# Performance work log

Hardware: AMD Instinct MI355X
Metric: run time of the kernel (lower is better)

Reference implementation:

```python
import jax, jax.numpy as jnp
import numpy as np
from jax.scipy.special import logsumexp

N = 4096          # nodes per graph
E = 65536         # edges per graph
HID = 128
HEADS = 4
HD = HID // HEADS
L_GNN = 2
L_CROSS = 3
SINK_ITERS = 20
LN_EPS = 1e-5
SCALE = 1.0 / np.sqrt(HD)


def layer_norm(x, g, b):
    m = jnp.mean(x, axis=-1, keepdims=True)
    v = jnp.mean((x - m) ** 2, axis=-1, keepdims=True)
    return (x - m) * jax.lax.rsqrt(v + LN_EPS) * g + b


def gcn_conv(x, ei, w, b):
    # PyG GCNConv: self-loops + symmetric normalization, sum aggregation
    n = x.shape[0]
    xl = x @ w                                  # [n, hid]
    loops = jnp.arange(n, dtype=ei.dtype)
    src = jnp.concatenate([ei[0], loops])
    dst = jnp.concatenate([ei[1], loops])
    deg = jax.ops.segment_sum(jnp.ones_like(src, dtype=x.dtype), dst, num_segments=n)
    dinv = jnp.where(deg > 0, jax.lax.rsqrt(deg), 0.0)
    norm = dinv[src] * dinv[dst]                # [E+n]
    msg = xl[src] * norm[:, None]
    return jax.ops.segment_sum(msg, dst, num_segments=n) + b


def encode(x, ei, gcn_w, gcn_b, ln_g, ln_b):
    h = x
    for l in range(L_GNN):
        h = gcn_conv(h, ei, gcn_w[l], gcn_b[l])
        h = layer_norm(h, ln_g[l], ln_b[l])
        h = jax.nn.relu(h)
    return h


def attend(X, Y, wq, wk, wv, wo, bo):
    # X attends to Y; residual add
    n, m = X.shape[0], Y.shape[0]
    Q = (X @ wq).reshape(n, HEADS, HD).transpose(1, 0, 2)   # [h, n, d]
    K = (Y @ wk).reshape(m, HEADS, HD).transpose(1, 0, 2)
    V = (Y @ wv).reshape(m, HEADS, HD).transpose(1, 0, 2)
    scores = jnp.einsum('hnd,hmd->hnm', Q, K) * SCALE
    attn = jax.nn.softmax(scores, axis=-1)
    O = jnp.einsum('hnm,hmd->hnd', attn, V)                 # [h, n, d]
    O = O.transpose(1, 0, 2).reshape(n, HID)
    return O @ wo + bo + X


def sinkhorn(log_alpha, n_iters=SINK_ITERS):
    def body(i, lp):
        lp = lp - logsumexp(lp, axis=1, keepdims=True)  # row normalize
        lp = lp - logsumexp(lp, axis=0, keepdims=True)  # col normalize
        return lp
    log_p = jax.lax.fori_loop(0, n_iters, body, log_alpha)
    return jnp.exp(log_p)


def setup_inputs() -> dict:
    key = jax.random.key(0)
    ks = jax.random.split(key, 24)
    f32 = jnp.float32
    w = lambda k, *s: jax.random.normal(k, s, dtype=f32) * 0.05
    inp = {
        'A_x': jax.random.normal(ks[0], (N, HID), dtype=f32),
        'A_ei': jax.random.randint(ks[1], (2, E), 0, N),
        'B_x': jax.random.normal(ks[2], (N, HID), dtype=f32),
        'B_ei': jax.random.randint(ks[3], (2, E), 0, N),
        'in_proj_w': w(ks[4], HID, HID),
        'in_proj_b': jnp.zeros((HID,), f32),
        'gcn_w': w(ks[5], L_GNN, HID, HID),
        'gcn_b': jnp.zeros((L_GNN, HID), f32),
        'gcn_ln_g': jnp.ones((L_GNN, HID), f32),
        'gcn_ln_b': jnp.zeros((L_GNN, HID), f32),
        'cross_q': w(ks[6], L_CROSS, HID, HID),
        'cross_k': w(ks[7], L_CROSS, HID, HID),
        'cross_v': w(ks[8], L_CROSS, HID, HID),
        'cross_o': w(ks[9], L_CROSS, HID, HID),
        'cross_o_b': jnp.zeros((L_CROSS, HID), f32),
        'post_ln_g': jnp.ones((HID,), f32),
        'post_ln_b': jnp.zeros((HID,), f32),
        'proj_w': w(ks[10], HID, HID),
        'proj_b': jnp.zeros((HID,), f32),
        'null_vec': jax.random.normal(ks[11], (HID,), dtype=f32) * 0.01,
        'cp_w1': w(ks[12], HID, HID),
        'cp_b1': jnp.zeros((HID,), f32),
        'cp_w2': w(ks[13], HID, HID),
        'cp_b2': jnp.zeros((HID,), f32),
    }
    return inp


def reference(A_x, A_ei, B_x, B_ei, in_proj_w, in_proj_b, gcn_w, gcn_b,
              gcn_ln_g, gcn_ln_b, cross_q, cross_k, cross_v, cross_o,
              cross_o_b, post_ln_g, post_ln_b, proj_w, proj_b, null_vec,
              cp_w1, cp_b1, cp_w2, cp_b2):
    A_in = A_x @ in_proj_w + in_proj_b
    B_in = B_x @ in_proj_w + in_proj_b
    A_h = encode(A_in, A_ei, gcn_w, gcn_b, gcn_ln_g, gcn_ln_b)
    B_h = encode(B_in, B_ei, gcn_w, gcn_b, gcn_ln_g, gcn_ln_b)
    for l in range(L_CROSS):
        A_new = attend(A_h, B_h, cross_q[l], cross_k[l], cross_v[l], cross_o[l], cross_o_b[l])
        B_new = attend(B_h, A_h, cross_q[l], cross_k[l], cross_v[l], cross_o[l], cross_o_b[l])
        A_h, B_h = A_new, B_new
    A_h = layer_norm(A_h, post_ln_g, post_ln_b)
    B_h = layer_norm(B_h, post_ln_g, post_ln_b)
    A_p = A_h @ proj_w + proj_b
    B_p = B_h @ proj_w + proj_b
    inv_sqrt_d = 1.0 / np.sqrt(HID)
    logits = (A_p @ B_p.T) * inv_sqrt_d                    # [N, N]
    null_col = (A_p @ null_vec) * inv_sqrt_d               # [N]
    logits_with_null = jnp.concatenate([logits, null_col[:, None]], axis=1)
    P = sinkhorn(logits_with_null)
    zA = jax.nn.relu(A_p @ cp_w1 + cp_b1) @ cp_w2 + cp_b2
    zB = jax.nn.relu(B_p @ cp_w1 + cp_b1) @ cp_w2 + cp_b2
    return (logits_with_null, P, zA, zB)
```

## Files before the change

kernel.cpp:

```cpp
#include <hip/hip_runtime.h>
#include <hip/hip_bf16.h>
#include <math.h>

#define NN 4096
#define EE 65536
#define HID_ 128
#define HDIM 32
#define NCOL 4097
#define EHP 4104

static constexpr float SCALE_ATT = 0.17677669529663687f;
static constexpr float INV_SQRT_D = 0.08838834764831845f;
static constexpr float LOG2E = 1.4426950408889634f;

typedef __attribute__((ext_vector_type(8))) short bf16x8;
typedef __attribute__((ext_vector_type(4))) float f32x4;
typedef _Float16 half8 __attribute__((ext_vector_type(8)));
typedef _Float16 half4v __attribute__((ext_vector_type(4)));

__device__ __forceinline__ float wred64(float v) {
#pragma unroll
  for (int m = 32; m > 0; m >>= 1) v += __shfl_xor(v, m, 64);
  return v;
}

__device__ __forceinline__ ushort f2b(float f) {
  __hip_bfloat16 h = __float2bfloat16(f);
  union { __hip_bfloat16 h; ushort u; } c;
  c.h = h;
  return c.u;
}

__device__ __forceinline__ unsigned pack2bf(float e0, float e1) {
  return ((__float_as_uint(e1) + 0x8000u) & 0xffff0000u) |
         ((__float_as_uint(e0) + 0x8000u) >> 16);
}

__global__ void wprep_k(const float* __restrict__ in_w,
                        const float* __restrict__ gcn_w,
                        const float* __restrict__ cq,
                        const float* __restrict__ ck,
                        const float* __restrict__ cv,
                        const float* __restrict__ co,
                        const float* __restrict__ pw,
                        const float* __restrict__ w1,
                        const float* __restrict__ w2, ushort* __restrict__ wth,
                        ushort* __restrict__ wtl) {
  int s = blockIdx.y;
  const float* W = s == 0    ? in_w
                   : s < 3   ? gcn_w + (size_t)(s - 1) * 16384
                   : s < 6   ? cq + (size_t)(s - 3) * 16384
                   : s < 9   ? ck + (size_t)(s - 6) * 16384
                   : s < 12  ? cv + (size_t)(s - 9) * 16384
                   : s < 15  ? co + (size_t)(s - 12) * 16384
                   : s == 15 ? pw
                   : s == 16 ? w1
                             : w2;
  int n0 = blockIdx.x * 16;
  int tid = threadIdx.x;
#pragma unroll
  for (int i = 0; i < 8; ++i) {
    int idx = tid + i * 256;
    int k = idx & 127, nn = idx >> 7;
    float v = W[(size_t)k * 128 + n0 + nn];
    ushort h = f2b(v);
    float hf = __uint_as_float((unsigned)h << 16);
    ushort lo = f2b(v - hf);
    size_t o = (size_t)s * 16384 + (size_t)(n0 + nn) * 128 + k;
    wth[o] = h;
    wtl[o] = lo;
  }
}

template <bool BIAS, bool RELU, bool RESID, bool BF16OUT, bool COMBINE>
__global__ __launch_bounds__(256) void gemm_mfma_k(
    const float* __restrict__ x0, const float* __restrict__ x1,
    const float* __restrict__ lp, const ushort* __restrict__ wth,
    const ushort* __restrict__ wtl, const float* __restrict__ bias,
    const float* __restrict__ res0, const float* __restrict__ res1,
    float* __restrict__ o0, float* __restrict__ o1, ushort* __restrict__ ob0,
    ushort* __restrict__ ob1) {
  __shared__ ushort Xh[32 * 128], Xl[32 * 128];
  __shared__ ushort Whs[64 * 128], Wls[64 * 128];
  const int tid = threadIdx.x;
  const int dir = blockIdx.y;
  const int m0 = blockIdx.x * 32;
  const float* res = dir ? res1 : res0;
  float* out = dir ? o1 : o0;
  ushort* outb = dir ? ob1 : ob0;

  {
    const float* x = dir ? x1 : x0;
#pragma unroll
    for (int i = 0; i < 2; ++i) {
      int c = tid + i * 256;
      int row = c >> 4, ch = c & 15;
      int rowg = m0 + row;
      float v[8];
      if (COMBINE) {
        int hh = ch >> 2;
        float ls = lp[((size_t)(dir * 4 + hh)) * NN + rowg] +
                   lp[((size_t)((2 + dir) * 4 + hh)) * NN + rowg];
        float inv = 1.f / ls;
        const float* p0 = &x0[((size_t)dir * NN + rowg) * HID_ + ch * 8];
        const float* p1 = &x0[((size_t)(2 + dir) * NN + rowg) * HID_ + ch * 8];
        float4 a0 = *(const float4*)p0, a1 = *(const float4*)(p0 + 4);
        float4 b0 = *(const float4*)p1, b1 = *(const float4*)(p1 + 4);
        v[0] = (a0.x + b0.x) * inv; v[1] = (a0.y + b0.y) * inv;
        v[2] = (a0.z + b0.z) * inv; v[3] = (a0.w + b0.w) * inv;
        v[4] = (a1.x + b1.x) * inv; v[5] = (a1.y + b1.y) * inv;
        v[6] = (a1.z + b1.z) * inv; v[7] = (a1.w + b1.w) * inv;
      } else {
        float4 a0 = *(const float4*)&x[(size_t)rowg * HID_ + ch * 8];
        float4 a1 = *(const float4*)&x[(size_t)rowg * HID_ + ch * 8 + 4];
        v[0] = a0.x; v[1] = a0.y; v[2] = a0.z; v[3] = a0.w;
        v[4] = a1.x; v[5] = a1.y; v[6] = a1.z; v[7] = a1.w;
      }
      union { ushort u[8]; bf16x8 vv; } H, L;
#pragma unroll
      for (int e = 0; e < 8; ++e) {
        ushort h = f2b(v[e]);
        float hf = __uint_as_float((unsigned)h << 16);
        H.u[e] = h;
        L.u[e] = f2b(v[e] - hf);
      }
      int pch = ch ^ (row & 15);
      *(bf16x8*)&Xh[row * 128 + pch * 8] = H.vv;
      *(bf16x8*)&Xl[row * 128 + pch * 8] = L.vv;
    }
  }

  const int w = tid >> 6, l = tid & 63, lr = l & 15, lg = l >> 4;
  const int mrow = (w & 1) * 16 + lr;
  const int nb = (w >> 1) * 2;

#pragma unroll
  for (int nh = 0; nh < 2; ++nh) {
    if (nh) __syncthreads();
#pragma unroll
    for (int i = 0; i < 4; ++i) {
      int c = tid + i * 256;
      int row = c >> 4, ch = c & 15;
      int pch = ch ^ (row & 15);
      *(bf16x8*)&Whs[row * 128 + pch * 8] =
          *(const bf16x8*)&wth[(size_t)(nh * 64 + row) * 128 + ch * 8];
      *(bf16x8*)&Wls[row * 128 + pch * 8] =
          *(const bf16x8*)&wtl[(size_t)(nh * 64 + row) * 128 + ch * 8];
    }
    __syncthreads();
    f32x4 acc0 = {0.f, 0.f, 0.f, 0.f}, acc1 = {0.f, 0.f, 0.f, 0.f};
#pragma unroll
    for (int kc = 0; kc < 4; ++kc) {
      int chx = ((kc * 4 + lg) ^ lr) * 8;
      bf16x8 ah = *(const bf16x8*)&Xh[mrow * 128 + chx];
      bf16x8 al = *(const bf16x8*)&Xl[mrow * 128 + chx];
      bf16x8 bh0 = *(const bf16x8*)&Whs[(nb * 16 + lr) * 128 + chx];
      bf16x8 bl0 = *(const bf16x8*)&Wls[(nb * 16 + lr) * 128 + chx];
      bf16x8 bh1 = *(const bf16x8*)&Whs[((nb + 1) * 16 + lr) * 128 + chx];
      bf16x8 bl1 = *(const bf16x8*)&Wls[((nb + 1) * 16 + lr) * 128 + chx];
      acc0 = __builtin_amdgcn_mfma_f32_16x16x32_bf16(ah, bh0, acc0, 0, 0, 0);
      acc0 = __builtin_amdgcn_mfma_f32_16x16x32_bf16(al, bh0, acc0, 0, 0, 0);
      acc0 = __builtin_amdgcn_mfma_f32_16x16x32_bf16(ah, bl0, acc0, 0, 0, 0);
      acc1 = __builtin_amdgcn_mfma_f32_16x16x32_bf16(ah, bh1, acc1, 0, 0, 0);
      acc1 = __builtin_amdgcn_mfma_f32_16x16x32_bf16(al, bh1, acc1, 0, 0, 0);
      acc1 = __builtin_amdgcn_mfma_f32_16x16x32_bf16(ah, bl1, acc1, 0, 0, 0);
    }
#pragma unroll
    for (int j = 0; j < 2; ++j) {
      const f32x4 a = j ? acc1 : acc0;
      int col = nh * 64 + (nb + j) * 16 + lr;
      float bv = BIAS ? bias[col] : 0.f;
#pragma unroll
      for (int r = 0; r < 4; ++r) {
        int rowg = m0 + (w & 1) * 16 + lg * 4 + r;
        float val = a[r] + bv;
        if (RESID) val += res[(size_t)rowg * HID_ + col];
        if (RELU) val = fmaxf(val, 0.f);
        out[(size_t)rowg * HID_ + col] = val;
        if (BF16OUT) outb[(size_t)rowg * HID_ + col] = f2b(val);
      }
    }
  }
}

__global__ __launch_bounds__(256) void gemm_qkv_mfma_k(
    const float* __restrict__ x0, const float* __restrict__ x1,
    const ushort* __restrict__ wthQ, const ushort* __restrict__ wtlQ,
    const ushort* __restrict__ wthK, const ushort* __restrict__ wtlK,
    const ushort* __restrict__ wthV, const ushort* __restrict__ wtlV,
    ushort* __restrict__ QA, ushort* __restrict__ QB, ushort* __restrict__ KA,
    ushort* __restrict__ KB, ushort* __restrict__ VA,
    ushort* __restrict__ VB) {
  __shared__ ushort Xh[32 * 128], Xl[32 * 128];
  __shared__ ushort Whs[64 * 128], Wls[64 * 128];
  const int tid = threadIdx.x;
  const int dir = blockIdx.y, z = blockIdx.z;
  const int m0 = blockIdx.x * 32;
  const ushort* wth = z == 0 ? wthQ : (z == 1 ? wthK : wthV);
  const ushort* wtl = z == 0 ? wtlQ : (z == 1 ? wtlK : wtlV);
  ushort* out = z == 0 ? (dir ? QB : QA)
                       : (z == 1 ? (dir ? KB : KA) : (dir ? VB : VA));
  const float scale = (z == 0) ? SCALE_ATT * LOG2E : 1.f;
  {
    const float* x = dir ? x1 : x0;
#pragma unroll
    for (int i = 0; i < 2; ++i) {
      int c = tid + i * 256;
      int row = c >> 4, ch = c & 15;
      int rowg = m0 + row;
      float4 a0 = *(const float4*)&x[(size_t)rowg * HID_ + ch * 8];
      float4 a1 = *(const float4*)&x[(size_t)rowg * HID_ + ch * 8 + 4];
      float v[8] = {a0.x, a0.y, a0.z, a0.w, a1.x, a1.y, a1.z, a1.w};
      union { ushort u[8]; bf16x8 vv; } H, L;
#pragma unroll
      for (int e = 0; e < 8; ++e) {
        ushort h = f2b(v[e]);
        float hf = __uint_as_float((unsigned)h << 16);
        H.u[e] = h;
        L.u[e] = f2b(v[e] - hf);
      }
      int pch = ch ^ (row & 15);
      *(bf16x8*)&Xh[row * 128 + pch * 8] = H.vv;
      *(bf16x8*)&Xl[row * 128 + pch * 8] = L.vv;
    }
  }
  const int w = tid >> 6, l = tid & 63, lr = l & 15, lg = l >> 4;
  const int mrow = (w & 1) * 16 + lr;
  const int nb = (w >> 1) * 2;
#pragma unroll
  for (int nh = 0; nh < 2; ++nh) {
    if (nh) __syncthreads();
#pragma unroll
    for (int i = 0; i < 4; ++i) {
      int c = tid + i * 256;
      int row = c >> 4, ch = c & 15;
      int pch = ch ^ (row & 15);
      *(bf16x8*)&Whs[row * 128 + pch * 8] =
          *(const bf16x8*)&wth[(size_t)(nh * 64 + row) * 128 + ch * 8];
      *(bf16x8*)&Wls[row * 128 + pch * 8] =
          *(const bf16x8*)&wtl[(size_t)(nh * 64 + row) * 128 + ch * 8];
    }
    __syncthreads();
    f32x4 acc0 = {0.f, 0.f, 0.f, 0.f}, acc1 = {0.f, 0.f, 0.f, 0.f};
#pragma unroll
    for (int kc = 0; kc < 4; ++kc) {
      int chx = ((kc * 4 + lg) ^ lr) * 8;
      bf16x8 ah = *(const bf16x8*)&Xh[mrow * 128 + chx];
      bf16x8 al = *(const bf16x8*)&Xl[mrow * 128 + chx];
      bf16x8 bh0 = *(const bf16x8*)&Whs[(nb * 16 + lr) * 128 + chx];
      bf16x8 bl0 = *(const bf16x8*)&Wls[(nb * 16 + lr) * 128 + chx];
      bf16x8 bh1 = *(const bf16x8*)&Whs[((nb + 1) * 16 + lr) * 128 + chx];
      bf16x8 bl1 = *(const bf16x8*)&Wls[((nb + 1) * 16 + lr) * 128 + chx];
      acc0 = __builtin_amdgcn_mfma_f32_16x16x32_bf16(ah, bh0, acc0, 0, 0, 0);
      acc0 = __builtin_amdgcn_mfma_f32_16x16x32_bf16(al, bh0, acc0, 0, 0, 0);
      acc0 = __builtin_amdgcn_mfma_f32_16x16x32_bf16(ah, bl0, acc0, 0, 0, 0);
      acc1 = __builtin_amdgcn_mfma_f32_16x16x32_bf16(ah, bh1, acc1, 0, 0, 0);
      acc1 = __builtin_amdgcn_mfma_f32_16x16x32_bf16(al, bh1, acc1, 0, 0, 0);
      acc1 = __builtin_amdgcn_mfma_f32_16x16x32_bf16(ah, bl1, acc1, 0, 0, 0);
    }
#pragma unroll
    for (int j = 0; j < 2; ++j) {
      const f32x4 a = j ? acc1 : acc0;
      int col = nh * 64 + (nb + j) * 16 + lr;
#pragma unroll
      for (int r = 0; r < 4; ++r) {
        int rowg = m0 + (w & 1) * 16 + lg * 4 + r;
        if (z < 2)
          out[(size_t)rowg * HID_ + col] = f2b(a[r] * scale);
        else
          out[(size_t)col * NN + rowg] = f2b(a[r]);
      }
    }
  }
}

__global__ void count_deg_k(const int* __restrict__ eiA,
                            const int* __restrict__ eiB, int* cntA, int* cntB) {
  int e = blockIdx.x * 256 + threadIdx.x;
  const int* ei = blockIdx.y ? eiB : eiA;
  int* cnt = blockIdx.y ? cntB : cntA;
  atomicAdd(&cnt[ei[EE + e]], 1);
}

__global__ __launch_bounds__(1024) void scan_k(const int* cntA, const int* cntB,
                                               int* rpA, int* rpB, float* dinvA,
                                               float* dinvB) {
  const int* cnt = blockIdx.y ? cntB : cntA;
  int* rp = blockIdx.y ? rpB : rpA;
  float* dinv = blockIdx.y ? dinvB : dinvA;
  __shared__ int part[1024];
  int tid = threadIdx.x;
  int v0 = cnt[tid * 4], v1 = cnt[tid * 4 + 1], v2 = cnt[tid * 4 + 2],
      v3 = cnt[tid * 4 + 3];
  int tot = v0 + v1 + v2 + v3;
  part[tid] = tot;
  __syncthreads();
  int x = tot;
  for (int off = 1; off < 1024; off <<= 1) {
    int y = (tid >= off) ? part[tid - off] : 0;
    __syncthreads();
    x += y;
    part[tid] = x;
    __syncthreads();
  }
  int excl = x - tot;
  rp[tid * 4] = excl;
  rp[tid * 4 + 1] = excl + v0;
  rp[tid * 4 + 2] = excl + v0 + v1;
  rp[tid * 4 + 3] = excl + v0 + v1 + v2;
  if (tid == 1023) rp[4096] = x;
  dinv[tid * 4] = rsqrtf((float)(v0 + 1));
  dinv[tid * 4 + 1] = rsqrtf((float)(v1 + 1));
  dinv[tid * 4 + 2] = rsqrtf((float)(v2 + 1));
  dinv[tid * 4 + 3] = rsqrtf((float)(v3 + 1));
}

__global__ void fill_k(const int* __restrict__ eiA, const int* __restrict__ eiB,
                       const int* rpA, const int* rpB, int* fillA, int* fillB,
                       int* srcA, int* srcB) {
  int e = blockIdx.x * 256 + threadIdx.x;
  const int* ei = blockIdx.y ? eiB : eiA;
  const int* rp = blockIdx.y ? rpB : rpA;
  int* fill = blockIdx.y ? fillB : fillA;
  int* src = blockIdx.y ? srcB : srcA;
  int d = ei[EE + e], s = ei[e];
  int pos = atomicAdd(&fill[d], 1);
  src[rp[d] + pos] = s;
}

__global__ __launch_bounds__(256) void gcn_agg_k(
    const float* __restrict__ xlA, const float* __restrict__ xlB,
    const int* __restrict__ rpA, const int* __restrict__ rpB,
    const int* __restrict__ srcA, const int* __restrict__ srcB,
    const float* __restrict__ dinvA, const float* __restrict__ dinvB,
    const float* __restrict__ gb, const float* __restrict__ lg,
    const float* __restrict__ lb, float* __restrict__ outA,
    float* __restrict__ outB) {
  const float* xl = blockIdx.y ? xlB : xlA;
  const int* rp = blockIdx.y ? rpB : rpA;
  const int* src = blockIdx.y ? srcB : srcA;
  const float* dinv = blockIdx.y ? dinvB : dinvA;
  float* out = blockIdx.y ? outB : outA;
  int wid = threadIdx.x >> 6, lane = threadIdx.x & 63;
  int node = blockIdx.x * 4 + wid;
  int b = rp[node], e = rp[node + 1];
  float di = dinv[node];
  float a0 = 0.f, a1 = 0.f;
  for (int base = b; base < e; base += 64) {
    int rem = e - base;
    int sv = 0;
    float wv = 0.f;
    if (lane < rem) {
      int s = src[base + lane];
      sv = s;
      wv = dinv[s] * di;
    }
    int nch = rem < 64 ? rem : 64;
    for (int j = 0; j < nch; ++j) {
      int s = __shfl(sv, j, 64);
      float w = __shfl(wv, j, 64);
      a0 += xl[(size_t)s * HID_ + lane] * w;
      a1 += xl[(size_t)s * HID_ + 64 + lane] * w;
    }
  }
  a0 += xl[(size_t)node * HID_ + lane] * di * di;
  a1 += xl[(size_t)node * HID_ + 64 + lane] * di * di;
  a0 += gb[lane];
  a1 += gb[64 + lane];
  float mean = wred64(a0 + a1) * (1.f / 128.f);
  float d0 = a0 - mean, d1 = a1 - mean;
  float var = wred64(d0 * d0 + d1 * d1) * (1.f / 128.f);
  float rs = rsqrtf(var + 1e-5f);
  float o0 = d0 * rs * lg[lane] + lb[lane];
  float o1 = d1 * rs * lg[64 + lane] + lb[64 + lane];
  out[(size_t)node * HID_ + lane] = fmaxf(o0, 0.f);
  out[(size_t)node * HID_ + 64 + lane] = fmaxf(o1, 0.f);
}

__global__ __launch_bounds__(256) void ln_k(float* __restrict__ hA,
                                            float* __restrict__ hB,
                                            const float* __restrict__ g,
                                            const float* __restrict__ b) {
  float* h = blockIdx.y ? hB : hA;
  int wid = threadIdx.x >> 6, lane = threadIdx.x & 63;
  int row = blockIdx.x * 4 + wid;
  float a0 = h[(size_t)row * HID_ + lane];
  float a1 = h[(size_t)row * HID_ + 64 + lane];
  float mean = wred64(a0 + a1) * (1.f / 128.f);
  float d0 = a0 - mean, d1 = a1 - mean;
  float var = wred64(d0 * d0 + d1 * d1) * (1.f / 128.f);
  float rs = rsqrtf(var + 1e-5f);
  h[(size_t)row * HID_ + lane] = d0 * rs * g[lane] + b[lane];
  h[(size_t)row * HID_ + 64 + lane] = d1 * rs * g[64 + lane] + b[64 + lane];
}

__global__ __launch_bounds__(256, 4) void attn_mfma_k(
    const ushort* __restrict__ QA, const ushort* __restrict__ KA,
    const ushort* __restrict__ VtA, const ushort* __restrict__ QB,
    const ushort* __restrict__ KB, const ushort* __restrict__ VtB,
    float* __restrict__ Opart, float* __restrict__ lpart) {
  const int qt = blockIdx.x, h = blockIdx.y;
  const int dir = blockIdx.z >> 1, sl = blockIdx.z & 1;
  const ushort* Q = dir ? QB : QA;
  const ushort* K = dir ? KA : KB;
  const ushort* Vt = dir ? VtA : VtB;

  __shared__ ushort KF[2048];
  __shared__ ushort VF[2048];
  __shared__ ushort PF[4][1024];

  const int tid = threadIdx.x;
  const int w = tid >> 6, l = tid & 63;
  const int lr = l & 15, lg = l >> 4;

  const int qrow = qt * 64 + w * 16 + lr;
  bf16x8 qf = *(const bf16x8*)&Q[(size_t)qrow * HID_ + h * HDIM + lg * 8];

  f32x4 oacc0 = {0.f, 0.f, 0.f, 0.f};
  f32x4 oacc1 = {0.f, 0.f, 0.f, 0.f};
  float lsum = 0.f;

  const int ldst = ((w * 4 + lg) * 16 + lr) * 8;
  const ushort* Kg =
      K + (size_t)(sl * 2048 + w * 16 + lr) * HID_ + h * HDIM + lg * 8;
  const ushort* Vg = Vt + (size_t)(h * HDIM + (w >> 1) * 16 + lr) * NN +
                     sl * 2048 + (w & 1) * 32 + lg * 8;

  bf16x8 kreg = *(const bf16x8*)Kg;
  bf16x8 vreg = *(const bf16x8*)Vg;

  for (int t = 0; t < 32; ++t) {
    __syncthreads();
    *(bf16x8*)&KF[ldst] = kreg;
    *(bf16x8*)&VF[ldst] = vreg;
    if (t < 31) {
      kreg = *(const bf16x8*)&Kg[(size_t)(t + 1) * 64 * HID_];
      vreg = *(const bf16x8*)&Vg[(t + 1) * 64];
    }
    __syncthreads();
#pragma unroll
    for (int s = 0; s < 4; ++s) {
      bf16x8 kf = *(const bf16x8*)&KF[((s * 4 + lg) * 16 + lr) * 8];
      f32x4 c = {0.f, 0.f, 0.f, 0.f};
      c = __builtin_amdgcn_mfma_f32_16x16x32_bf16(kf, qf, c, 0, 0, 0);
      float e0 = exp2f(c[0]), e1 = exp2f(c[1]);
      float e2 = exp2f(c[2]), e3 = exp2f(c[3]);
      lsum += (e0 + e1) + (e2 + e3);
      const int k0 = s >> 1;
      const int lgr = (s & 1) * 2 + (lg >> 1);
      const int e8 = (lg & 1) * 4;
      *(uint2*)&PF[w][((k0 * 4 + lgr) * 16 + lr) * 8 + e8] =
          make_uint2(pack2bf(e0, e1), pack2bf(e2, e3));
    }
#pragma unroll
    for (int k0 = 0; k0 < 2; ++k0) {
      bf16x8 pa = *(const bf16x8*)&PF[w][((k0 * 4 + lg) * 16 + lr) * 8];
      bf16x8 vb0 = *(const bf16x8*)&VF[((k0 * 4 + lg) * 16 + lr) * 8];
      bf16x8 vb1 = *(const bf16x8*)&VF[(((2 + k0) * 4 + lg) * 16 + lr) * 8];
      oacc0 = __builtin_amdgcn_mfma_f32_16x16x32_bf16(pa, vb0, oacc0, 0, 0, 0);
      oacc1 = __builtin_amdgcn_mfma_f32_16x16x32_bf16(pa, vb1, oacc1, 0, 0, 0);
    }
  }
  lsum += __shfl_xor(lsum, 16, 64);
  lsum += __shfl_xor(lsum, 32, 64);
  const int pb = sl * 2 + dir;
  if (lg == 0)
    lpart[(size_t)(pb * 4 + h) * NN + qt * 64 + w * 16 + lr] = lsum;
#pragma unroll
  for (int r = 0; r < 4; ++r) {
    int q = qt * 64 + w * 16 + lg * 4 + r;
    Opart[((size_t)pb * NN + q) * HID_ + h * HDIM + lr] = oacc0[r];
    Opart[((size_t)pb * NN + q) * HID_ + h * HDIM + 16 + lr] = oacc1[r];
  }
}

__global__ __launch_bounds__(256, 2) void gemm_nt_mfma_k(
    const ushort* __restrict__ Apb, const ushort* __restrict__ Bpb,
    float* __restrict__ L, _Float16* __restrict__ Eh) {
  __shared__ ushort As[128 * 128];
  __shared__ ushort Bs[128 * 128];
  const int tid = threadIdx.x;
  const int ab = blockIdx.y * 128, bb = blockIdx.x * 128;
#pragma unroll
  for (int i = 0; i < 8; ++i) {
    int lin = tid + i * 256;
    int row = lin >> 4, ch = lin & 15;
    int pch = ch ^ (row & 15);
    *(bf16x8*)&As[row * 128 + pch * 8] =
        *(const bf16x8*)&Apb[(size_t)(ab + row) * HID_ + ch * 8];
    *(bf16x8*)&Bs[row * 128 + pch * 8] =
        *(const bf16x8*)&Bpb[(size_t)(bb + row) * HID_ + ch * 8];
  }
  __syncthreads();
  const int w = tid >> 6, l = tid & 63, lr = l & 15, lg = l >> 4;
  f32x4 acc[2][8];
#pragma unroll
  for (int fm = 0; fm < 2; ++fm)
#pragma unroll
    for (int nf = 0; nf < 8; ++nf) acc[fm][nf] = {0.f, 0.f, 0.f, 0.f};
#pragma unroll
  for (int kc = 0; kc < 4; ++kc) {
    bf16x8 a0 = *(const bf16x8*)
        &As[((w * 2 + 0) * 16 + lr) * 128 + ((kc * 4 + lg) ^ lr) * 8];
    bf16x8 a1 = *(const bf16x8*)
        &As[((w * 2 + 1) * 16 + lr) * 128 + ((kc * 4 + lg) ^ lr) * 8];
#pragma unroll
    for (int nf = 0; nf < 8; ++nf) {
      bf16x8 bf = *(const bf16x8*)
          &Bs[(nf * 16 + lr) * 128 + ((kc * 4 + lg) ^ lr) * 8];
      acc[0][nf] = __builtin_amdgcn_mfma_f32_16x16x32_bf16(a0, bf, acc[0][nf], 0, 0, 0);
      acc[1][nf] = __builtin_amdgcn_mfma_f32_16x16x32_bf16(a1, bf, acc[1][nf], 0, 0, 0);
    }
  }
#pragma unroll
  for (int fm = 0; fm < 2; ++fm)
#pragma unroll
    for (int nf = 0; nf < 8; ++nf)
#pragma unroll
      for (int r = 0; r < 4; ++r) {
        int row = ab + (w * 2 + fm) * 16 + lg * 4 + r;
        int col = bb + nf * 16 + lr;
        float v = acc[fm][nf][r] * INV_SQRT_D;
        L[(size_t)row * NCOL + col] = v;
        Eh[(size_t)row * EHP + col] = (_Float16)exp2f(v * LOG2E);
      }
}

__global__ void null_col_k(const float* __restrict__ Ap,
                           const float* __restrict__ nv, float* __restrict__ L,
                           _Float16* __restrict__ Eh) {
  int row = blockIdx.x, lane = threadIdx.x;
  float s = Ap[(size_t)row * HID_ + lane] * nv[lane] +
            Ap[(size_t)row * HID_ + 64 + lane] * nv[64 + lane];
  s = wred64(s);
  if (lane == 0) {
    float v = s * INV_SQRT_D;
    L[(size_t)row * NCOL + 4096] = v;
    Eh[(size_t)row * EHP + 4096] = (_Float16)exp2f(v * LOG2E);
  }
  if (lane >= 1 && lane < 8) Eh[(size_t)row * EHP + 4096 + lane] = (_Float16)0.f;
}

__global__ __launch_bounds__(256) void sink_fused_k(
    const _Float16* __restrict__ Eh, const float* __restrict__ t_old,
    float* __restrict__ t_new, float* __restrict__ colpart,
    float* __restrict__ u) {
  __shared__ float vinv[EHP];
  __shared__ float uls[16];
  const int tid = threadIdx.x, bid = blockIdx.x;
  if (bid < 17) {
    int z = bid * 256 + tid;
    if (z < EHP) t_new[z] = 0.f;
  }
  for (int i = tid; i < EHP; i += 256)
    vinv[i] = (i < NCOL) ? (1.f / t_old[i]) : 0.f;
  __syncthreads();
  const int w = tid >> 6, l = tid & 63;
  const int row0 = bid * 16;
#pragma unroll
  for (int rr = 0; rr < 4; ++rr) {
    int row = row0 + w * 4 + rr;
    const _Float16* Ep = Eh + (size_t)row * EHP;
    float s = 0.f;
    for (int j = l * 4; j < EHP; j += 256) {
      half4v e = *(const half4v*)&Ep[j];
      float4 vv = *(const float4*)&vinv[j];
      s += (float)e[0] * vv.x + (float)e[1] * vv.y + (float)e[2] * vv.z +
           (float)e[3] * vv.w;
    }
    s = wred64(s);
    if (l == 0) {
      float uv = 1.f / s;
      uls[w * 4 + rr] = uv;
      u[row] = uv;
    }
  }
  __syncthreads();
  float ur[16];
#pragma unroll
  for (int r = 0; r < 16; ++r) ur[r] = uls[r];
  float* cp = colpart + (size_t)bid * EHP;
  for (int j = tid * 4; j < EHP; j += 1024) {
    float a0 = 0.f, a1 = 0.f, a2 = 0.f, a3 = 0.f;
#pragma unroll
    for (int r = 0; r < 16; ++r) {
      half4v e = *(const half4v*)&Eh[(size_t)(row0 + r) * EHP + j];
      a0 += (float)e[0] * ur[r];
      a1 += (float)e[1] * ur[r];
      a2 += (float)e[2] * ur[r];
      a3 += (float)e[3] * ur[r];
    }
    *(float4*)&cp[j] = make_float4(a0, a1, a2, a3);
  }
}

__global__ __launch_bounds__(256) void sink_reduce_k(
    const float* __restrict__ colpart, float* __restrict__ t_new) {
  int j = blockIdx.x * 256 + threadIdx.x;
  if (j >= EHP) return;
  int b0 = blockIdx.y * 32;
  float s = 0.f;
#pragma unroll 8
  for (int b = 0; b < 32; ++b) s += colpart[(size_t)(b0 + b) * EHP + j];
  atomicAdd(&t_new[j], s);
}

__global__ void sink_init_k(float* t0) {
  int j = blockIdx.x * 256 + threadIdx.x;
  if (j < EHP) t0[j] = 1.f;
}

__global__ __launch_bounds__(256) void sink_finalE_k(
    const _Float16* __restrict__ Eh, const float* __restrict__ u,
    const float* __restrict__ t, float* __restrict__ P) {
  __shared__ float vls[NCOL];
  int tid = threadIdx.x, row = blockIdx.x;
  for (int i = tid; i < NCOL; i += 256) vls[i] = 1.f / t[i];
  __syncthreads();
  float ur = u[row];
  const _Float16* Ep = Eh + (size_t)row * EHP;
  float* Pp = P + (size_t)row * NCOL;
  for (int j = tid; j < NCOL; j += 256) Pp[j] = (float)Ep[j] * ur * vls[j];
}

extern "C" void kernel_launch(void* const* d_in, const int* in_sizes, int n_in,
                              void* d_out, int out_size, void* d_ws,
                              size_t ws_size, hipStream_t stream) {
  const float* A_x = (const float*)d_in[0];
  const int* A_ei = (const int*)d_in[1];
  const float* B_x = (const float*)d_in[2];
  const int* B_ei = (const int*)d_in[3];
  const float* in_w = (const float*)d_in[4];
  const float* in_b = (const float*)d_in[5];
  const float* gcn_w = (const float*)d_in[6];
  const float* gcn_b = (const float*)d_in[7];
  const float* lng = (const float*)d_in[8];
  const float* lnb = (const float*)d_in[9];
  const float* cq = (const float*)d_in[10];
  const float* ck = (const float*)d_in[11];
  const float* cv = (const float*)d_in[12];
  const float* co = (const float*)d_in[13];
  const float* cob = (const float*)d_in[14];
  const float* plg = (const float*)d_in[15];
  const float* plb = (const float*)d_in[16];
  const float* pw = (const float*)d_in[17];
  const float* pb = (const float*)d_in[18];
  const float* nullv = (const float*)d_in[19];
  const float* w1 = (const float*)d_in[20];
  const float* b1 = (const float*)d_in[21];
  const float* w2 = (const float*)d_in[22];
  const float* b2 = (const float*)d_in[23];

  float* ws = (float*)d_ws;
  size_t off = 0;
  auto alloc = [&](size_t n) { float* p = ws + off; off += n; return p; };
  const size_t NHE = (size_t)NN * HID_;
  float* tA = alloc(NHE);
  float* tB = alloc(NHE);
  float* Ap = alloc(NHE);
  float* Bp = alloc(NHE);
  ushort* Apb = (ushort*)alloc(NHE / 2);
  ushort* Bpb = (ushort*)alloc(NHE / 2);
  ushort* WThi = (ushort*)alloc((size_t)18 * 16384 / 2);
  ushort* WTlo = (ushort*)alloc((size_t)18 * 16384 / 2);
  float* uvec = alloc(NN);
  float* t0 = alloc(EHP);
  float* t1 = alloc(EHP);
  float* zone = ws + off;
  float* hA0 = alloc(NHE); float* hB0 = alloc(NHE);
  float* hA1 = alloc(NHE); float* hB1 = alloc(NHE);
  float* QA = alloc(NHE);  float* KAb = alloc(NHE); float* VAb = alloc(NHE);
  float* QB = alloc(NHE);  float* KBb = alloc(NHE); float* VBb = alloc(NHE);
  float* Opart = alloc(4 * NHE);
  float* lpart = alloc((size_t)16 * NN);
  float* dinvA = alloc(NN); float* dinvB = alloc(NN);
  int* ib = (int*)(ws + off);
  int* cntA = ib;             int* cntB = cntA + NN;
  int* fillA = cntB + NN;     int* fillB = fillA + NN;
  int* rpA = fillB + NN;      int* rpB = rpA + (NN + 1);
  int* srcA = rpB + (NN + 1); int* srcB = srcA + EE;
  size_t ints_floats = (size_t)(4 * NN + 2 * (NN + 1) + 2 * EE);
  _Float16* Eh = (_Float16*)zone;
  {
    size_t named = (size_t)((ws + off) - zone) + ints_floats;
    size_t eh_floats = ((size_t)NN * EHP + 1) / 2;
    size_t need = eh_floats > named ? eh_floats : named;
    off = (size_t)(zone - ws) + need;
  }
  float* colpart = alloc((size_t)256 * EHP);

  float* Lout = (float*)d_out;
  float* Pout = Lout + (size_t)NN * NCOL;
  float* zA = Pout + (size_t)NN * NCOL;
  float* zB = zA + NHE;

  hipMemsetAsync(cntA, 0, 4 * NN * sizeof(int), stream);

  wprep_k<<<dim3(8, 18), 256, 0, stream>>>(in_w, gcn_w, cq, ck, cv, co, pw, w1,
                                           w2, WThi, WTlo);
  gemm_mfma_k<true, false, false, false, false>
      <<<dim3(128, 2), 256, 0, stream>>>(A_x, B_x, nullptr, WThi, WTlo, in_b,
                                         nullptr, nullptr, hA0, hB0, nullptr,
                                         nullptr);
  count_deg_k<<<dim3(256, 2), 256, 0, stream>>>(A_ei, B_ei, cntA, cntB);
  scan_k<<<dim3(1, 2), 1024, 0, stream>>>(cntA, cntB, rpA, rpB, dinvA, dinvB);
  fill_k<<<dim3(256, 2), 256, 0, stream>>>(A_ei, B_ei, rpA, rpB, fillA, fillB,
                                           srcA, srcB);
  float* hA = hA0; float* hB = hB0; float* aA = hA1; float* aB = hB1;
  for (int l = 0; l < 2; ++l) {
    gemm_mfma_k<false, false, false, false, false>
        <<<dim3(128, 2), 256, 0, stream>>>(
            hA, hB, nullptr, WThi + (size_t)16384 * (1 + l),
            WTlo + (size_t)16384 * (1 + l), nullptr, nullptr, nullptr, tA, tB,
            nullptr, nullptr);
    gcn_agg_k<<<dim3(1024, 2), 256, 0, stream>>>(
        tA, tB, rpA, rpB, srcA, srcB, dinvA, dinvB, gcn_b + l * HID_,
        lng + l * HID_, lnb + l * HID_, hA, hB);
  }
  for (int l = 0; l < 3; ++l) {
    gemm_qkv_mfma_k<<<dim3(128, 2, 3), 256, 0, stream>>>(
        hA, hB, WThi + (size_t)16384 * (3 + l), WTlo + (size_t)16384 * (3 + l),
        WThi + (size_t)16384 * (6 + l), WTlo + (size_t)16384 * (6 + l),
        WThi + (size_t)16384 * (9 + l), WTlo + (size_t)16384 * (9 + l),
        (ushort*)QA, (ushort*)QB, (ushort*)KAb, (ushort*)KBb, (ushort*)VAb,
        (ushort*)VBb);
    attn_mfma_k<<<dim3(64, 4, 4), 256, 0, stream>>>(
        (ushort*)QA, (ushort*)KAb, (ushort*)VAb, (ushort*)QB, (ushort*)KBb,
        (ushort*)VBb, Opart, lpart);
    gemm_mfma_k<true, false, true, false, true>
        <<<dim3(128, 2), 256, 0, stream>>>(
            Opart, nullptr, lpart, WThi + (size_t)16384 * (12 + l),
            WTlo + (size_t)16384 * (12 + l), cob + l * HID_, hA, hB, aA, aB,
            nullptr, nullptr);
    float* t;
    t = hA; hA = aA; aA = t;
    t = hB; hB = aB; aB = t;
  }
  ln_k<<<dim3(1024, 2), 256, 0, stream>>>(hA, hB, plg, plb);
  gemm_mfma_k<true, false, false, true, false>
      <<<dim3(128, 2), 256, 0, stream>>>(hA, hB, nullptr,
                                         WThi + (size_t)16384 * 15,
                                         WTlo + (size_t)16384 * 15, pb, nullptr,
                                         nullptr, Ap, Bp, Apb, Bpb);
  gemm_nt_mfma_k<<<dim3(32, 32), 256, 0, stream>>>(Apb, Bpb, Lout, Eh);
  null_col_k<<<NN, 64, 0, stream>>>(Ap, nullv, Lout, Eh);
  sink_init_k<<<17, 256, 0, stream>>>(t0);
  float* tb[2] = {t0, t1};
  for (int it = 0; it < 20; ++it) {
    float* told = tb[it & 1];
    float* tnew = tb[(it + 1) & 1];
    sink_fused_k<<<256, 256, 0, stream>>>(Eh, told, tnew, colpart, uvec);
    sink_reduce_k<<<dim3(17, 8), 256, 0, stream>>>(colpart, tnew);
  }
  sink_finalE_k<<<NN, 256, 0, stream>>>(Eh, uvec, tb[0], Pout);
  gemm_mfma_k<true, true, false, false, false>
      <<<dim3(128, 2), 256, 0, stream>>>(Ap, Bp, nullptr,
                                         WThi + (size_t)16384 * 16,
                                         WTlo + (size_t)16384 * 16, b1, nullptr,
                                         nullptr, tA, tB, nullptr, nullptr);
  gemm_mfma_k<true, false, false, false, false>
      <<<dim3(128, 2), 256, 0, stream>>>(tA, tB, nullptr,
                                         WThi + (size_t)16384 * 17,
                                         WTlo + (size_t)16384 * 17, b2, nullptr,
                                         nullptr, zA, zB, nullptr, nullptr);
}
```

Before: 1.079 ms.

## Fuse Sinkhorn column reduction via replicated atomics and widen attention key split

Each Sinkhorn iteration now uses one kernel instead of two. Column sums are accumulated with atomics into 8 replicated accumulator buffers, rotated through three buffers so one can be zeroed while the others are read. This removes the colpart staging buffer and the separate reduce launch, at the cost of atomic contention and readers summing 8 replicas. Attention splits the key range into 4 slices instead of 2, with a higher occupancy hint to add parallelism, and the combine step sums 4 partials. The bf16 hi/lo split is also rewritten with integer rounding arithmetic.

```diff
diff --git a/kernel.cpp b/kernel.cpp
--- a/kernel.cpp
+++ b/kernel.cpp
@@ -8,6 +8,7 @@
 #define HDIM 32
 #define NCOL 4097
 #define EHP 4104
+#define NREP 8
 
 static constexpr float SCALE_ATT = 0.17677669529663687f;
 static constexpr float INV_SQRT_D = 0.08838834764831845f;
@@ -15,7 +16,6 @@
 
 typedef __attribute__((ext_vector_type(8))) short bf16x8;
 typedef __attribute__((ext_vector_type(4))) float f32x4;
-typedef _Float16 half8 __attribute__((ext_vector_type(8)));
 typedef _Float16 half4v __attribute__((ext_vector_type(4)));
 
 __device__ __forceinline__ float wred64(float v) {
@@ -34,6 +34,13 @@
 __device__ __forceinline__ unsigned pack2bf(float e0, float e1) {
   return ((__float_as_uint(e1) + 0x8000u) & 0xffff0000u) |
          ((__float_as_uint(e0) + 0x8000u) >> 16);
+}
+
+__device__ __forceinline__ void split2(float v, ushort& h, ushort& l) {
+  unsigned hb = (__float_as_uint(v) + 0x8000u) & 0xffff0000u;
+  h = (ushort)(hb >> 16);
+  float lo = v - __uint_as_float(hb);
+  l = (ushort)((__float_as_uint(lo) + 0x8000u) >> 16);
 }
 
 __global__ void wprep_k(const float* __restrict__ in_w,
@@ -63,9 +70,8 @@
     int idx = tid + i * 256;
     int k = idx & 127, nn = idx >> 7;
     float v = W[(size_t)k * 128 + n0 + nn];
-    ushort h = f2b(v);
-    float hf = __uint_as_float((unsigned)h << 16);
-    ushort lo = f2b(v - hf);
+    ushort h, lo;
+    split2(v, h, lo);
     size_t o = (size_t)s * 16384 + (size_t)(n0 + nn) * 128 + k;
     wth[o] = h;
     wtl[o] = lo;
@@ -99,17 +105,23 @@
       float v[8];
       if (COMBINE) {
         int hh = ch >> 2;
-        float ls = lp[((size_t)(dir * 4 + hh)) * NN + rowg] +
-                   lp[((size_t)((2 + dir) * 4 + hh)) * NN + rowg];
+        float ls = 0.f;
+#pragma unroll
+        for (int sl = 0; sl < 4; ++sl)
+          ls += lp[((size_t)((sl * 2 + dir) * 4 + hh)) * NN + rowg];
         float inv = 1.f / ls;
-        const float* p0 = &x0[((size_t)dir * NN + rowg) * HID_ + ch * 8];
-        const float* p1 = &x0[((size_t)(2 + dir) * NN + rowg) * HID_ + ch * 8];
-        float4 a0 = *(const float4*)p0, a1 = *(const float4*)(p0 + 4);
-        float4 b0 = *(const float4*)p1, b1 = *(const float4*)(p1 + 4);
-        v[0] = (a0.x + b0.x) * inv; v[1] = (a0.y + b0.y) * inv;
-        v[2] = (a0.z + b0.z) * inv; v[3] = (a0.w + b0.w) * inv;
-        v[4] = (a1.x + b1.x) * inv; v[5] = (a1.y + b1.y) * inv;
-        v[6] = (a1.z + b1.z) * inv; v[7] = (a1.w + b1.w) * inv;
+#pragma unroll
+        for (int e = 0; e < 8; ++e) v[e] = 0.f;
+#pragma unroll
+        for (int sl = 0; sl < 4; ++sl) {
+          const float* p =
+              &x0[((size_t)(sl * 2 + dir) * NN + rowg) * HID_ + ch * 8];
+          float4 a0 = *(const float4*)p, a1 = *(const float4*)(p + 4);
+          v[0] += a0.x; v[1] += a0.y; v[2] += a0.z; v[3] += a0.w;
+          v[4] += a1.x; v[5] += a1.y; v[6] += a1.z; v[7] += a1.w;
+        }
+#pragma unroll
+        for (int e = 0; e < 8; ++e) v[e] *= inv;
       } else {
         float4 a0 = *(const float4*)&x[(size_t)rowg * HID_ + ch * 8];
         float4 a1 = *(const float4*)&x[(size_t)rowg * HID_ + ch * 8 + 4];
@@ -118,12 +130,7 @@
       }
       union { ushort u[8]; bf16x8 vv; } H, L;
 #pragma unroll
-      for (int e = 0; e < 8; ++e) {
-        ushort h = f2b(v[e]);
-        float hf = __uint_as_float((unsigned)h << 16);
-        H.u[e] = h;
-        L.u[e] = f2b(v[e] - hf);
-      }
+      for (int e = 0; e < 8; ++e) split2(v[e], H.u[e], L.u[e]);
       int pch = ch ^ (row & 15);
       *(bf16x8*)&Xh[row * 128 + pch * 8] = H.vv;
       *(bf16x8*)&Xl[row * 128 + pch * 8] = L.vv;
@@ -213,12 +220,7 @@
       float v[8] = {a0.x, a0.y, a0.z, a0.w, a1.x, a1.y, a1.z, a1.w};
       union { ushort u[8]; bf16x8 vv; } H, L;
 #pragma unroll
-      for (int e = 0; e < 8; ++e) {
-        ushort h = f2b(v[e]);
-        float hf = __uint_as_float((unsigned)h << 16);
-        H.u[e] = h;
-        L.u[e] = f2b(v[e] - hf);
-      }
+      for (int e = 0; e < 8; ++e) split2(v[e], H.u[e], L.u[e]);
       int pch = ch ^ (row & 15);
       *(bf16x8*)&Xh[row * 128 + pch * 8] = H.vv;
       *(bf16x8*)&Xl[row * 128 + pch * 8] = L.vv;
@@ -394,13 +396,13 @@
   h[(size_t)row * HID_ + 64 + lane] = d1 * rs * g[64 + lane] + b[64 + lane];
 }
 
-__global__ __launch_bounds__(256, 4) void attn_mfma_k(
+__global__ __launch_bounds__(256, 8) void attn_mfma_k(
     const ushort* __restrict__ QA, const ushort* __restrict__ KA,
     const ushort* __restrict__ VtA, const ushort* __restrict__ QB,
     const ushort* __restrict__ KB, const ushort* __restrict__ VtB,
     float* __restrict__ Opart, float* __restrict__ lpart) {
   const int qt = blockIdx.x, h = blockIdx.y;
-  const int dir = blockIdx.z >> 1, sl = blockIdx.z & 1;
+  const int dir = blockIdx.z >> 2, sl = blockIdx.z & 3;
   const ushort* Q = dir ? QB : QA;
   const ushort* K = dir ? KA : KB;
   const ushort* Vt = dir ? VtA : VtB;
@@ -422,18 +424,18 @@
 
   const int ldst = ((w * 4 + lg) * 16 + lr) * 8;
   const ushort* Kg =
-      K + (size_t)(sl * 2048 + w * 16 + lr) * HID_ + h * HDIM + lg * 8;
+      K + (size_t)(sl * 1024 + w * 16 + lr) * HID_ + h * HDIM + lg * 8;
   const ushort* Vg = Vt + (size_t)(h * HDIM + (w >> 1) * 16 + lr) * NN +
-                     sl * 2048 + (w & 1) * 32 + lg * 8;
+                     sl * 1024 + (w & 1) * 32 + lg * 8;
 
   bf16x8 kreg = *(const bf16x8*)Kg;
   bf16x8 vreg = *(const bf16x8*)Vg;
 
-  for (int t = 0; t < 32; ++t) {
+  for (int t = 0; t < 16; ++t) {
     __syncthreads();
     *(bf16x8*)&KF[ldst] = kreg;
     *(bf16x8*)&VF[ldst] = vreg;
-    if (t < 31) {
+    if (t < 15) {
       kreg = *(const bf16x8*)&Kg[(size_t)(t + 1) * 64 * HID_];
       vreg = *(const bf16x8*)&Vg[(t + 1) * 64];
     }
@@ -541,19 +543,23 @@
   if (lane >= 1 && lane < 8) Eh[(size_t)row * EHP + 4096 + lane] = (_Float16)0.f;
 }
 
-__global__ __launch_bounds__(256) void sink_fused_k(
+__global__ __launch_bounds__(256) void sink_iter_k(
     const _Float16* __restrict__ Eh, const float* __restrict__ t_old,
-    float* __restrict__ t_new, float* __restrict__ colpart,
+    float* __restrict__ t_new, float* __restrict__ t_zero,
     float* __restrict__ u) {
   __shared__ float vinv[EHP];
   __shared__ float uls[16];
   const int tid = threadIdx.x, bid = blockIdx.x;
-  if (bid < 17) {
+  {
     int z = bid * 256 + tid;
-    if (z < EHP) t_new[z] = 0.f;
-  }
-  for (int i = tid; i < EHP; i += 256)
-    vinv[i] = (i < NCOL) ? (1.f / t_old[i]) : 0.f;
+    if (z < NREP * EHP) t_zero[z] = 0.f;
+  }
+  for (int i = tid; i < EHP; i += 256) {
+    float s = 0.f;
+#pragma unroll
+    for (int r = 0; r < NREP; ++r) s += t_old[r * EHP + i];
+    vinv[i] = (i < NCOL) ? (1.f / s) : 0.f;
+  }
   __syncthreads();
   const int w = tid >> 6, l = tid & 63;
   const int row0 = bid * 16;
@@ -579,7 +585,7 @@
   float ur[16];
 #pragma unroll
   for (int r = 0; r < 16; ++r) ur[r] = uls[r];
-  float* cp = colpart + (size_t)bid * EHP;
+  float* trep = t_new + (size_t)(bid & (NREP - 1)) * EHP;
   for (int j = tid * 4; j < EHP; j += 1024) {
     float a0 = 0.f, a1 = 0.f, a2 = 0.f, a3 = 0.f;
 #pragma unroll
@@ -590,24 +596,19 @@
       a2 += (float)e[2] * ur[r];
       a3 += (float)e[3] * ur[r];
     }
-    *(float4*)&cp[j] = make_float4(a0, a1, a2, a3);
-  }
-}
-
-__global__ __launch_bounds__(256) void sink_reduce_k(
-    const float* __restrict__ colpart, float* __restrict__ t_new) {
-  int j = blockIdx.x * 256 + threadIdx.x;
-  if (j >= EHP) return;
-  int b0 = blockIdx.y * 32;
-  float s = 0.f;
-#pragma unroll 8
-  for (int b = 0; b < 32; ++b) s += colpart[(size_t)(b0 + b) * EHP + j];
-  atomicAdd(&t_new[j], s);
-}
-
-__global__ void sink_init_k(float* t0) {
-  int j = blockIdx.x * 256 + threadIdx.x;
-  if (j < EHP) t0[j] = 1.f;
+    atomicAdd(&trep[j + 0], a0);
+    atomicAdd(&trep[j + 1], a1);
+    atomicAdd(&trep[j + 2], a2);
+    atomicAdd(&trep[j + 3], a3);
+  }
+}
+
+__global__ void sink_init_k(float* t0, float* t1) {
+  int z = blockIdx.x * 256 + threadIdx.x;
+  if (z < NREP * EHP) {
+    t0[z] = (z < EHP) ? 1.f : 0.f;
+    t1[z] = 0.f;
+  }
 }
 
 __global__ __launch_bounds__(256) void sink_finalE_k(
@@ -615,7 +616,12 @@
     const float* __restrict__ t, float* __restrict__ P) {
   __shared__ float vls[NCOL];
   int tid = threadIdx.x, row = blockIdx.x;
-  for (int i = tid; i < NCOL; i += 256) vls[i] = 1.f / t[i];
+  for (int i = tid; i < NCOL; i += 256) {
+    float s = 0.f;
+#pragma unroll
+    for (int r = 0; r < NREP; ++r) s += t[r * EHP + i];
+    vls[i] = 1.f / s;
+  }
   __syncthreads();
   float ur = u[row];
   const _Float16* Ep = Eh + (size_t)row * EHP;
@@ -664,15 +670,16 @@
   ushort* WThi = (ushort*)alloc((size_t)18 * 16384 / 2);
   ushort* WTlo = (ushort*)alloc((size_t)18 * 16384 / 2);
   float* uvec = alloc(NN);
-  float* t0 = alloc(EHP);
-  float* t1 = alloc(EHP);
+  float* t0 = alloc((size_t)NREP * EHP);
+  float* t1 = alloc((size_t)NREP * EHP);
+  float* t2 = alloc((size_t)NREP * EHP);
   float* zone = ws + off;
   float* hA0 = alloc(NHE); float* hB0 = alloc(NHE);
   float* hA1 = alloc(NHE); float* hB1 = alloc(NHE);
   float* QA = alloc(NHE);  float* KAb = alloc(NHE); float* VAb = alloc(NHE);
   float* QB = alloc(NHE);  float* KBb = alloc(NHE); float* VBb = alloc(NHE);
-  float* Opart = alloc(4 * NHE);
-  float* lpart = alloc((size_t)16 * NN);
+  float* Opart = alloc(8 * NHE);
+  float* lpart = alloc((size_t)32 * NN);
   float* dinvA = alloc(NN); float* dinvB = alloc(NN);
   int* ib = (int*)(ws + off);
   int* cntA = ib;             int* cntB = cntA + NN;
@@ -687,7 +694,6 @@
     size_t need = eh_floats > named ? eh_floats : named;
     off = (size_t)(zone - ws) + need;
   }
-  float* colpart = alloc((size_t)256 * EHP);
 
   float* Lout = (float*)d_out;
   float* Pout = Lout + (size_t)NN * NCOL;
@@ -724,7 +730,7 @@
         WThi + (size_t)16384 * (9 + l), WTlo + (size_t)16384 * (9 + l),
         (ushort*)QA, (ushort*)QB, (ushort*)KAb, (ushort*)KBb, (ushort*)VAb,
         (ushort*)VBb);
-    attn_mfma_k<<<dim3(64, 4, 4), 256, 0, stream>>>(
+    attn_mfma_k<<<dim3(64, 4, 8), 256, 0, stream>>>(
         (ushort*)QA, (ushort*)KAb, (ushort*)VAb, (ushort*)QB, (ushort*)KBb,
         (ushort*)VBb, Opart, lpart);
     gemm_mfma_k<true, false, true, false, true>
@@ -744,15 +750,13 @@
                                          nullptr, Ap, Bp, Apb, Bpb);
   gemm_nt_mfma_k<<<dim3(32, 32), 256, 0, stream>>>(Apb, Bpb, Lout, Eh);
   null_col_k<<<NN, 64, 0, stream>>>(Ap, nullv, Lout, Eh);
-  sink_init_k<<<17, 256, 0, stream>>>(t0);
-  float* tb[2] = {t0, t1};
+  sink_init_k<<<129, 256, 0, stream>>>(t0, t1);
+  float* tb[3] = {t0, t1, t2};
   for (int it = 0; it < 20; ++it) {
-    float* told = tb[it & 1];
-    float* tnew = tb[(it + 1) & 1];
-    sink_fused_k<<<256, 256, 0, stream>>>(Eh, told, tnew, colpart, uvec);
-    sink_reduce_k<<<dim3(17, 8), 256, 0, stream>>>(colpart, tnew);
-  }
-  sink_finalE_k<<<NN, 256, 0, stream>>>(Eh, uvec, tb[0], Pout);
+    sink_iter_k<<<256, 256, 0, stream>>>(Eh, tb[it % 3], tb[(it + 1) % 3],
+                                         tb[(it + 2) % 3], uvec);
+  }
+  sink_finalE_k<<<NN, 256, 0, stream>>>(Eh, uvec, tb[2], Pout);
   gemm_mfma_k<true, true, false, false, false>
       <<<dim3(128, 2), 256, 0, stream>>>(Ap, Bp, nullptr,
                                          WThi + (size_t)16384 * 16,
```

Result: slower. 1.302 ms (+20.7%).
